# Performance work log

Measured on AMD Instinct MI355X. Metric: run time of the kernel, lower is better.

Reference implementation:

```python
import jax, jax.numpy as jnp
import numpy as np

B, L, E, H = 2, 2048, 1024, 16
D = E // H

def setup_inputs() -> dict:
    key = jax.random.key(0)
    ks = jax.random.split(key, 6)
    values = jax.random.normal(ks[0], (B, L, E), dtype=jnp.float32)
    keys = jax.random.normal(ks[1], (B, L, E), dtype=jnp.float32)
    query = jax.random.normal(ks[2], (B, L, E), dtype=jnp.float32)
    mask = jax.random.randint(ks[3], (B, 1, L, L), 0, 2, dtype=jnp.int32)
    W_out = jax.random.normal(ks[4], (E, E), dtype=jnp.float32) * 0.02
    b_out = jax.random.normal(ks[5], (E,), dtype=jnp.float32) * 0.02
    return {"values": values, "keys": keys, "query": query, "mask": mask,
            "W_out": W_out, "b_out": b_out}

def reference(values, keys, query, mask, W_out, b_out):
    # Note: source module never applies its per-head q/k/v Linear layers;
    # it only reshapes inputs, so we do the same.
    b, l, e = query.shape
    v = values.reshape(b, l, H, D)   # [B, K, H, D]
    k = keys.reshape(b, l, H, D)     # [B, K, H, D]
    q = query.reshape(b, l, H, D)    # [B, Q, H, D]
    # scores[b,h,q,k] = sum_d q[b,q,h,d] * k[b,k,h,d]
    scores = jnp.einsum('bqhd,bkhd->bhqk', q, k)
    scores = jnp.where(mask == 0, jnp.float32(-1e20), scores)
    # source scales by 1/sqrt(embed_size), not head_dim
    attn = jax.nn.softmax(scores / jnp.float32(E ** 0.5), axis=3)
    out = jnp.einsum('bhqk,bkhd->bqhd', attn, v).reshape(b, l, e)
    out = out @ W_out.T + b_out  # torch Linear: x @ W^T + b
    return out
```

## Files before the change

### kernel.cpp

```cpp
#include <hip/hip_runtime.h>
#include <hip/hip_bf16.h>

typedef __bf16 bf16;
typedef __bf16 bf16x8 __attribute__((ext_vector_type(8)));
typedef __bf16 bf16x4 __attribute__((ext_vector_type(4)));
typedef float  f32x4  __attribute__((ext_vector_type(4)));
typedef float  f32x16 __attribute__((ext_vector_type(16)));

#define B_ 2
#define L_ 2048
#define E_ 1024
#define H_ 16
#define D_ 64

__device__ __forceinline__ int swz(int r, int c) {
    return r * 64 + (((c ^ (r & 7)) & 7) << 3);
}

#define DMA16(gp, lp)                                                              \
    __builtin_amdgcn_global_load_lds(                                              \
        (const __attribute__((address_space(1))) unsigned int*)(gp),               \
        (__attribute__((address_space(3))) unsigned int*)(lp), 16, 0, 0)

__global__ __launch_bounds__(256) void prep_kernel(const float* __restrict__ v,
                                                   const float* __restrict__ keys,
                                                   const int* __restrict__ mask,
                                                   const float* __restrict__ W,
                                                   bf16* __restrict__ vt_,
                                                   bf16* __restrict__ kt_,
                                                   unsigned int* __restrict__ mtq2,
                                                   bf16* __restrict__ wbt) {
    __shared__ __attribute__((aligned(16))) float tile[64 * 65];
    const int bid = blockIdx.x;
    const int t = threadIdx.x;
    if (bid < 1024) {
        int bh = bid >> 5, b = bh >> 4, h = bh & 15, kt = bid & 31;
        int kk = t >> 2, dg = t & 3;
        const float* src = v + (((size_t)(b * L_ + kt * 64 + kk)) * H_ + h) * D_ + dg * 16;
        float4 f[4];
#pragma unroll
        for (int i = 0; i < 4; i++) f[i] = reinterpret_cast<const float4*>(src)[i];
#pragma unroll
        for (int i = 0; i < 16; i++)
            tile[(dg * 16 + i) * 65 + kk] = reinterpret_cast<const float*>(f)[i];
        __syncthreads();
        int dd = t >> 2, cg = t & 3;
        const int sig[16] = {0, 1, 2, 3, 8, 9, 10, 11, 4, 5, 6, 7, 12, 13, 14, 15};
        bf16 tmp[16];
#pragma unroll
        for (int p = 0; p < 16; p++)
            tmp[p] = (bf16)tile[dd * 65 + cg * 16 + sig[p]];
        bf16* dst = vt_ + ((size_t)bh * 32 + kt) * 4096;
        *reinterpret_cast<uint4*>(dst + swz(dd, cg * 2))     = *reinterpret_cast<const uint4*>(&tmp[0]);
        *reinterpret_cast<uint4*>(dst + swz(dd, cg * 2 + 1)) = *reinterpret_cast<const uint4*>(&tmp[8]);
    } else if (bid < 2048) {
        int idx = bid - 1024;
        int b = idx >> 9;
        int q = (idx & 511) * 4 + (t >> 6);
        int li = t & 63;
        const int* mrow = mask + ((size_t)b * L_ + q) * L_;
        unsigned int* mq = mtq2 + (size_t)b * 64 * 2048;
#pragma unroll 4
        for (int pass = 0; pass < 32; pass++) {
            int m = mrow[pass * 64 + li];
            unsigned long long bal = __ballot(m & 1);
            if (li == 0) mq[(size_t)(pass * 2) * 2048 + q] = (unsigned int)bal;
            if (li == 1) mq[(size_t)(pass * 2 + 1) * 2048 + q] = (unsigned int)(bal >> 32);
        }
    } else if (bid < 3072) {
        int idx = bid - 2048;
        int b = idx >> 9, h = (idx >> 5) & 15, kt = idx & 31;
        int r = t >> 2, cg = t & 3;
        const float* src = keys + ((size_t)(b * L_ + kt * 64 + r)) * E_ + h * 64 + cg * 16;
        float4 f[4];
#pragma unroll
        for (int i = 0; i < 4; i++) f[i] = reinterpret_cast<const float4*>(src)[i];
        bf16 tmp[16];
#pragma unroll
        for (int i = 0; i < 16; i++)
            tmp[i] = (bf16)reinterpret_cast<const float*>(f)[i];
        bf16* dst = kt_ + ((size_t)(b * 16 + h) * 32 + kt) * 4096;
        *reinterpret_cast<uint4*>(dst + swz(r, cg * 2))     = *reinterpret_cast<const uint4*>(&tmp[0]);
        *reinterpret_cast<uint4*>(dst + swz(r, cg * 2 + 1)) = *reinterpret_cast<const uint4*>(&tmp[8]);
    } else {
        int idx = bid - 3072;
        int n6 = idx >> 4, kt = idx & 15;
        int r = t >> 2, cg = t & 3;
        const float* src = W + ((size_t)(n6 * 64 + r)) * E_ + kt * 64 + cg * 16;
        float4 f[4];
#pragma unroll
        for (int i = 0; i < 4; i++) f[i] = reinterpret_cast<const float4*>(src)[i];
        bf16 tmp[16];
#pragma unroll
        for (int i = 0; i < 16; i++)
            tmp[i] = (bf16)reinterpret_cast<const float*>(f)[i];
        bf16* dst = wbt + ((size_t)(n6 * 16 + kt)) * 4096;
        *reinterpret_cast<uint4*>(dst + swz(r, cg * 2))     = *reinterpret_cast<const uint4*>(&tmp[0]);
        *reinterpret_cast<uint4*>(dst + swz(r, cg * 2 + 1)) = *reinterpret_cast<const uint4*>(&tmp[8]);
    }
}

__global__ __launch_bounds__(256, 4) void attn_kernel(const float* __restrict__ q_,
                                                      const bf16* __restrict__ kt_,
                                                      const bf16* __restrict__ vt_,
                                                      const unsigned int* __restrict__ mtq2,
                                                      bf16* __restrict__ xbt) {
    __shared__ __attribute__((aligned(16))) char smem[40960];
    bf16* Qs = (bf16*)(smem + 32768);
    float* Om = (float*)smem;
    float* Lrow = (float*)(smem + 16384);
    bf16* Xs = (bf16*)(smem + 16896);

    const int bh = blockIdx.y, b = bh >> 4, hd = bh & 15;
    const int q0 = blockIdx.x * 64;
    const int t = threadIdx.x;
    const int w = t >> 6, lane = t & 63, h = lane >> 5, l31 = lane & 31;
    const int wq = w & 1, wk = w >> 1;
    const int r_ = t >> 2, cg = t & 3;

    const float CSCALE = 1.4426950408889634f / 32.0f;

    const bf16* kbase = kt_ + (size_t)bh * 32 * 4096;
    const bf16* vbase = vt_ + (size_t)bh * 32 * 4096;

    {
        const bf16* gk = kbase + w * 1024 + lane * 8;
        DMA16(gk, smem + w * 2048);
        DMA16(gk + 512, smem + w * 2048 + 1024);
        const bf16* gv = vbase + w * 1024 + lane * 8;
        DMA16(gv, smem + 16384 + w * 2048);
        DMA16(gv + 512, smem + 16384 + w * 2048 + 1024);
    }
    {
        const float* src = q_ + ((size_t)(b * L_ + q0 + r_)) * E_ + hd * 64 + cg * 16;
        float4 f[4];
#pragma unroll
        for (int i = 0; i < 4; i++) f[i] = reinterpret_cast<const float4*>(src)[i];
        bf16 tmp[16];
#pragma unroll
        for (int i = 0; i < 16; i++)
            tmp[i] = (bf16)(reinterpret_cast<const float*>(f)[i] * CSCALE);
        *reinterpret_cast<uint4*>(&Qs[swz(r_, cg * 2)])     = *reinterpret_cast<const uint4*>(&tmp[0]);
        *reinterpret_cast<uint4*>(&Qs[swz(r_, cg * 2 + 1)]) = *reinterpret_cast<const uint4*>(&tmp[8]);
    }
    __syncthreads();

    bf16x8 bq[4];
#pragma unroll
    for (int dc = 0; dc < 4; dc++)
        bq[dc] = *reinterpret_cast<const bf16x8*>(&Qs[swz(wq * 32 + l31, dc * 2 + h)]);

    f32x16 oc[2] = {{}, {}};
    float lsum = 0.0f;

    const unsigned int* mbase = mtq2 + (size_t)b * 64 * 2048 + q0 + wq * 32 + l31;

    for (int kt = 0; kt < L_ / 64; kt++) {
        __syncthreads();
        bf16* Kc = (bf16*)(smem + (kt & 1) * 8192);
        bf16* Vc = (bf16*)(smem + 16384 + (kt & 1) * 8192);
        if (kt + 1 < L_ / 64) {
            char* Kn = smem + ((kt + 1) & 1) * 8192;
            char* Vn = smem + 16384 + ((kt + 1) & 1) * 8192;
            const bf16* gk = kbase + (size_t)(kt + 1) * 4096 + w * 1024 + lane * 8;
            DMA16(gk, Kn + w * 2048);
            DMA16(gk + 512, Kn + w * 2048 + 1024);
            const bf16* gv = vbase + (size_t)(kt + 1) * 4096 + w * 1024 + lane * 8;
            DMA16(gv, Vn + w * 2048);
            DMA16(gv + 512, Vn + w * 2048 + 1024);
        }
        unsigned int mw = mbase[(size_t)(kt * 2 + wk) * 2048];

        f32x16 st = {};
#pragma unroll
        for (int dc = 0; dc < 4; dc++) {
            bf16x8 ak = *reinterpret_cast<const bf16x8*>(&Kc[swz(wk * 32 + l31, dc * 2 + h)]);
            st = __builtin_amdgcn_mfma_f32_32x32x16_bf16(ak, bq[dc], st, 0, 0, 0);
        }

        const unsigned int mwh = mw >> (h * 4);
        bf16x8 bp[2];
        float pv[16];
#pragma unroll
        for (int i = 0; i < 16; i++) {
            const int base = (i & 3) + 8 * (i >> 2);
            float e = __builtin_amdgcn_exp2f(st[i]);
            pv[i] = ((mwh >> base) & 1u) ? e : 0.0f;
            lsum += pv[i];
        }
#pragma unroll
        for (int kc = 0; kc < 2; kc++)
#pragma unroll
            for (int j = 0; j < 8; j++)
                bp[kc][j] = (bf16)pv[kc * 8 + j];

#pragma unroll
        for (int da = 0; da < 2; da++)
#pragma unroll
            for (int kc = 0; kc < 2; kc++) {
                bf16x8 av = *reinterpret_cast<const bf16x8*>(&Vc[swz(da * 32 + l31, wk * 4 + kc * 2 + h)]);
                oc[da] = __builtin_amdgcn_mfma_f32_32x32x16_bf16(av, bp[kc], oc[da], 0, 0, 0);
            }
    }
    __syncthreads();

    float lw = lsum + __shfl(lsum, lane ^ 32, 64);
    if (wk == 1) {
#pragma unroll
        for (int da = 0; da < 2; da++)
#pragma unroll
            for (int i = 0; i < 16; i++) {
                int d = da * 32 + (i & 3) + 8 * (i >> 2) + 4 * h;
                Om[d * 64 + wq * 32 + l31] = oc[da][i];
            }
        if (h == 0) Lrow[wq * 32 + l31] = lw;
    }
    __syncthreads();
    if (wk == 0) {
        float rinv = 1.0f / (lw + Lrow[wq * 32 + l31]);
#pragma unroll
        for (int da = 0; da < 2; da++)
#pragma unroll
            for (int g = 0; g < 4; g++) {
                int d0 = da * 32 + 8 * g + 4 * h;
                bf16x4 pk;
#pragma unroll
                for (int r = 0; r < 4; r++)
                    pk[r] = (bf16)((oc[da][g * 4 + r] + Om[(d0 + r) * 64 + wq * 32 + l31]) * rinv);
                *reinterpret_cast<bf16x4*>(&Xs[(wq * 32 + l31) * 72 + d0]) = pk;
            }
    }
    __syncthreads();
    {
        bf16* xtile = xbt + ((size_t)((b * 32 + (q0 >> 6)) * 16 + hd)) * 4096;
        *reinterpret_cast<uint4*>(xtile + swz(r_, cg * 2))     = *reinterpret_cast<const uint4*>(&Xs[r_ * 72 + cg * 16]);
        *reinterpret_cast<uint4*>(xtile + swz(r_, cg * 2 + 1)) = *reinterpret_cast<const uint4*>(&Xs[r_ * 72 + cg * 16 + 8]);
    }
}

__global__ __launch_bounds__(256, 3) void proj_kernel(const bf16* __restrict__ xbt,
                                                      const bf16* __restrict__ wbt,
                                                      const float* __restrict__ bias,
                                                      float* __restrict__ out) {
    __shared__ __attribute__((aligned(16))) char smem[49152];
    const int n0 = blockIdx.x * 64, m0 = blockIdx.y * 128;
    const int t = threadIdx.x;
    const int w = t >> 6, lane = t & 63, h = lane >> 5, l31 = lane & 31;
    const int wm = w >> 1, wn = w & 1;

    const bf16* a0 = xbt + ((size_t)(m0 >> 6)) * 16 * 4096;
    const bf16* a1 = a0 + 16 * 4096;
    const bf16* bb_ = wbt + ((size_t)(n0 >> 6)) * 16 * 4096;

    {
#pragma unroll
        for (int i = 0; i < 4; i++) {
            int c = w * 4 + i;
            const bf16* g = ((c >> 3) ? a1 : a0) + (c & 7) * 512 + lane * 8;
            DMA16(g, smem + c * 1024);
        }
#pragma unroll
        for (int i = 0; i < 2; i++) {
            int c = w * 2 + i;
            DMA16(bb_ + c * 512 + lane * 8, smem + 32768 + c * 1024);
        }
    }

    f32x16 acc[2] = {{}, {}};
    for (int kt = 0; kt < E_ / 64; kt++) {
        __syncthreads();
        bf16* Ac = (bf16*)(smem + (kt & 1) * 16384);
        bf16* Bc = (bf16*)(smem + 32768 + (kt & 1) * 8192);
        if (kt + 1 < E_ / 64) {
            char* An = smem + ((kt + 1) & 1) * 16384;
            char* Bn = smem + 32768 + ((kt + 1) & 1) * 8192;
            const bf16* an0 = a0 + (kt + 1) * 4096;
            const bf16* an1 = a1 + (kt + 1) * 4096;
            const bf16* bn = bb_ + (kt + 1) * 4096;
#pragma unroll
            for (int i = 0; i < 4; i++) {
                int c = w * 4 + i;
                const bf16* g = ((c >> 3) ? an1 : an0) + (c & 7) * 512 + lane * 8;
                DMA16(g, An + c * 1024);
            }
#pragma unroll
            for (int i = 0; i < 2; i++) {
                int c = w * 2 + i;
                DMA16(bn + c * 512 + lane * 8, Bn + c * 1024);
            }
        }
#pragma unroll
        for (int dc = 0; dc < 4; dc++) {
            bf16x8 bfr = *reinterpret_cast<const bf16x8*>(&Bc[swz(wn * 32 + l31, dc * 2 + h)]);
#pragma unroll
            for (int mi = 0; mi < 2; mi++) {
                bf16x8 afr = *reinterpret_cast<const bf16x8*>(&Ac[wm * 4096 + swz(mi * 32 + l31, dc * 2 + h)]);
                acc[mi] = __builtin_amdgcn_mfma_f32_32x32x16_bf16(afr, bfr, acc[mi], 0, 0, 0);
            }
        }
    }

    float bv = bias[n0 + wn * 32 + l31];
#pragma unroll
    for (int mi = 0; mi < 2; mi++)
#pragma unroll
        for (int i = 0; i < 16; i++) {
            int row = m0 + wm * 64 + mi * 32 + (i & 3) + 8 * (i >> 2) + 4 * h;
            out[(size_t)row * E_ + n0 + wn * 32 + l31] = acc[mi][i] + bv;
        }
}

extern "C" void kernel_launch(void* const* d_in, const int* in_sizes, int n_in,
                              void* d_out, int out_size, void* d_ws, size_t ws_size,
                              hipStream_t stream) {
    (void)in_sizes; (void)n_in; (void)out_size; (void)ws_size;
    const float* values = (const float*)d_in[0];
    const float* keys   = (const float*)d_in[1];
    const float* query  = (const float*)d_in[2];
    const int*   mask   = (const int*)d_in[3];
    const float* W_out  = (const float*)d_in[4];
    const float* b_out  = (const float*)d_in[5];
    float* out = (float*)d_out;

    char* ws = (char*)d_ws;
    bf16* vt_ = (bf16*)(ws);
    bf16* kt_ = (bf16*)(ws + 8388608);
    bf16* wbt = (bf16*)(ws + 16777216);
    unsigned int* mtq2 = (unsigned int*)(ws + 18874368);
    bf16* xbt = (bf16*)(ws + 19922944);

    prep_kernel<<<3328, 256, 0, stream>>>(values, keys, mask, W_out, vt_, kt_, mtq2, wbt);
    attn_kernel<<<dim3(L_ / 64, B_ * H_), 256, 0, stream>>>(query, kt_, vt_, mtq2, xbt);
    proj_kernel<<<dim3(E_ / 64, (B_ * L_) / 128), 256, 0, stream>>>(xbt, wbt, b_out, out);
}
```

Measured before the change: 205.6 us.

## Vectorize mask packing, prefetch mask words, and branchless masking with MFMA priority

The mask-packing prep path now reads int4 per lane and builds a new interleaved bit layout, which cuts the number of passes and ballots. The attention loop loads the next tile's mask word one iteration ahead, so the global load latency overlaps the current tile's work. The per-element select is replaced by sign-extended bitmask ANDs and a two-lane vector sum of the row totals. s_setprio is raised around the MFMA blocks to favour matrix issue. The mask bit layout changes in both producer and consumer, so it must stay consistent between them.

Result: faster. 191.6 us, median of 2 (-6.8%).

```diff
diff --git a/kernel.cpp b/kernel.cpp
--- a/kernel.cpp
+++ b/kernel.cpp
@@ -4,6 +4,7 @@
 typedef __bf16 bf16;
 typedef __bf16 bf16x8 __attribute__((ext_vector_type(8)));
 typedef __bf16 bf16x4 __attribute__((ext_vector_type(4)));
+typedef float  f32x2  __attribute__((ext_vector_type(2)));
 typedef float  f32x4  __attribute__((ext_vector_type(4)));
 typedef float  f32x16 __attribute__((ext_vector_type(16)));
 
@@ -60,12 +61,20 @@
         int li = t & 63;
         const int* mrow = mask + ((size_t)b * L_ + q) * L_;
         unsigned int* mq = mtq2 + (size_t)b * 64 * 2048;
-#pragma unroll 4
-        for (int pass = 0; pass < 32; pass++) {
-            int m = mrow[pass * 64 + li];
-            unsigned long long bal = __ballot(m & 1);
-            if (li == 0) mq[(size_t)(pass * 2) * 2048 + q] = (unsigned int)bal;
-            if (li == 1) mq[(size_t)(pass * 2 + 1) * 2048 + q] = (unsigned int)(bal >> 32);
+#pragma unroll 2
+        for (int pass = 0; pass < 8; pass++) {
+            int4 m4 = reinterpret_cast<const int4*>(mrow)[pass * 64 + li];
+            unsigned long long b0 = __ballot(m4.x & 1);
+            unsigned long long b1 = __ballot(m4.y & 1);
+            unsigned long long b2 = __ballot(m4.z & 1);
+            unsigned long long b3 = __ballot(m4.w & 1);
+            if (li < 8) {
+                unsigned int word = (unsigned int)((b0 >> (8 * li)) & 0xFFull)
+                                  | ((unsigned int)((b1 >> (8 * li)) & 0xFFull) << 8)
+                                  | ((unsigned int)((b2 >> (8 * li)) & 0xFFull) << 16)
+                                  | ((unsigned int)((b3 >> (8 * li)) & 0xFFull) << 24);
+                mq[(size_t)(pass * 8 + li) * 2048 + q] = word;
+            }
         }
     } else if (bid < 3072) {
         int idx = bid - 2048;
@@ -151,9 +160,10 @@
         bq[dc] = *reinterpret_cast<const bf16x8*>(&Qs[swz(wq * 32 + l31, dc * 2 + h)]);
 
     f32x16 oc[2] = {{}, {}};
-    float lsum = 0.0f;
+    f32x2 ls = {0.0f, 0.0f};
 
     const unsigned int* mbase = mtq2 + (size_t)b * 64 * 2048 + q0 + wq * 32 + l31;
+    unsigned int mw = mbase[(size_t)wk * 2048];
 
     for (int kt = 0; kt < L_ / 64; kt++) {
         __syncthreads();
@@ -169,31 +179,40 @@
             DMA16(gv, Vn + w * 2048);
             DMA16(gv + 512, Vn + w * 2048 + 1024);
         }
-        unsigned int mw = mbase[(size_t)(kt * 2 + wk) * 2048];
+        unsigned int mw_nxt = (kt + 1 < L_ / 64)
+                                  ? mbase[(size_t)((kt + 1) * 2 + wk) * 2048] : 0u;
 
         f32x16 st = {};
+        __builtin_amdgcn_s_setprio(1);
 #pragma unroll
         for (int dc = 0; dc < 4; dc++) {
             bf16x8 ak = *reinterpret_cast<const bf16x8*>(&Kc[swz(wk * 32 + l31, dc * 2 + h)]);
             st = __builtin_amdgcn_mfma_f32_32x32x16_bf16(ak, bq[dc], st, 0, 0, 0);
         }
-
-        const unsigned int mwh = mw >> (h * 4);
+        __builtin_amdgcn_s_setprio(0);
+
+        const unsigned int mwh = mw >> h;
+        float pv[16];
+#pragma unroll
+        for (int i = 0; i < 16; i += 2) {
+            const int b0 = 8 * (i & 3) + 2 * (i >> 2);
+            const int b1 = 8 * ((i + 1) & 3) + 2 * ((i + 1) >> 2);
+            float e0 = __builtin_amdgcn_exp2f(st[i]);
+            float e1 = __builtin_amdgcn_exp2f(st[i + 1]);
+            int m0 = ((int)(mwh << (31 - b0))) >> 31;
+            int m1 = ((int)(mwh << (31 - b1))) >> 31;
+            pv[i]     = __int_as_float(__float_as_int(e0) & m0);
+            pv[i + 1] = __int_as_float(__float_as_int(e1) & m1);
+            ls += (f32x2){pv[i], pv[i + 1]};
+        }
         bf16x8 bp[2];
-        float pv[16];
-#pragma unroll
-        for (int i = 0; i < 16; i++) {
-            const int base = (i & 3) + 8 * (i >> 2);
-            float e = __builtin_amdgcn_exp2f(st[i]);
-            pv[i] = ((mwh >> base) & 1u) ? e : 0.0f;
-            lsum += pv[i];
-        }
 #pragma unroll
         for (int kc = 0; kc < 2; kc++)
 #pragma unroll
             for (int j = 0; j < 8; j++)
                 bp[kc][j] = (bf16)pv[kc * 8 + j];
 
+        __builtin_amdgcn_s_setprio(1);
 #pragma unroll
         for (int da = 0; da < 2; da++)
 #pragma unroll
@@ -201,9 +220,12 @@
                 bf16x8 av = *reinterpret_cast<const bf16x8*>(&Vc[swz(da * 32 + l31, wk * 4 + kc * 2 + h)]);
                 oc[da] = __builtin_amdgcn_mfma_f32_32x32x16_bf16(av, bp[kc], oc[da], 0, 0, 0);
             }
+        __builtin_amdgcn_s_setprio(0);
+        mw = mw_nxt;
     }
     __syncthreads();
 
+    float lsum = ls.x + ls.y;
     float lw = lsum + __shfl(lsum, lane ^ 32, 64);
     if (wk == 1) {
 #pragma unroll
```
